# Kernel tuning notes

Measured on AMD Instinct MI355X. Metric: run time of the kernel, lower is better.

## Reference

```python
import jax, jax.numpy as jnp
import numpy as np

DIM_HEAD = 64
NB_FEATURES = 256
COND_LEN = 128
NUM_CHUNKS = 128  # torch .chunk(128, dim=-2) -> 128 chunks
KERNEL_EPS = 1e-4
ATTN_EPS = 1e-6


def gaussian_orthogonal_random_matrix(key, nb_rows, nb_cols):
    # scaling == 0 branch of the torch code
    nb_full = nb_rows // nb_cols
    blocks = []
    for i in range(nb_full + (1 if nb_rows % nb_cols else 0)):
        g = jax.random.normal(jax.random.fold_in(key, i), (nb_cols, nb_cols), dtype=jnp.float32)
        qm, _ = jnp.linalg.qr(g)
        blocks.append(qm.T)
    final = jnp.concatenate(blocks, axis=0)[:nb_rows]
    mult = jnp.linalg.norm(
        jax.random.normal(jax.random.fold_in(key, 10_000), (nb_rows, nb_cols), dtype=jnp.float32), axis=1)
    return mult[:, None] * final  # diag(mult) @ final


def softmax_kernel(x, proj, is_query):
    d = x.shape[-1]
    data_normalizer = d ** (-0.25)
    ratio = proj.shape[0] ** (-0.5)
    # [b,h,n,m]
    data_dash = jnp.einsum('bhnd,md->bhnm', data_normalizer * x, proj)
    diag = (x * x).sum(-1) * 0.5 * (data_normalizer ** 2)  # [b,h,n]
    diag = diag[..., None]
    if is_query:
        m = jnp.max(data_dash, axis=-1, keepdims=True)
    else:
        m = jnp.max(data_dash)
    return ratio * (jnp.exp(data_dash - diag - m) + KERNEL_EPS)


def causal_linear_attention(qf, kf, v):
    b, h, s, m = qf.shape
    e = v.shape[-1]
    # conditioning prefix: non-causal linear attention
    cq, ck, cv = qf[:, :, :COND_LEN], kf[:, :, :COND_LEN], v[:, :, :COND_LEN]
    cond_k_sum = ck.sum(axis=-2)                                   # [b,h,m]
    cond_Dinv = 1.0 / jnp.einsum('bhnd,bhd->bhn', cq, cond_k_sum)
    cond_ctx = jnp.einsum('bhnd,bhne->bhde', ck, cv)               # [b,h,m,e]
    cond_out = jnp.einsum('bhde,bhnd,bhn->bhne', cond_ctx, cq, cond_Dinv)

    # causal chunked recurrence over the remainder
    rest = s - COND_LEN
    L = rest // NUM_CHUNKS
    def to_chunks(t):
        return t[:, :, COND_LEN:].reshape(b, h, NUM_CHUNKS, L, t.shape[-1]).transpose(2, 0, 1, 3, 4)
    qr, kr, vr = to_chunks(qf), to_chunks(kf), to_chunks(v)

    def step(carry, qkv):
        last_k, last_ctx = carry  # [b,h,m], [b,h,m,e]
        qc, kc, vc = qkv          # [b,h,L,m], [b,h,L,m], [b,h,L,e]
        k_cumsum = last_k[:, :, None, :] + jnp.cumsum(kc, axis=-2)
        D_inv = 1.0 / jnp.einsum('bhld,bhld->bhl', qc, k_cumsum + ATTN_EPS)
        ctx = jnp.einsum('bhld,bhle->bhlde', kc, vc)
        ctx_cumsum = last_ctx[:, :, None] + jnp.cumsum(ctx, axis=-3)
        out = jnp.einsum('bhlde,bhld,bhl->bhle', ctx_cumsum, qc, D_inv)
        return (k_cumsum[:, :, -1], ctx_cumsum[:, :, -1]), out

    _, outs = jax.lax.scan(step, (cond_k_sum, cond_ctx), (qr, kr, vr))
    outs = outs.transpose(1, 2, 0, 3, 4).reshape(b, h, rest, e)
    return jnp.concatenate([cond_out, outs], axis=2)


def setup_inputs() -> dict:
    key = jax.random.key(0)
    kq, kk, kv, kp = jax.random.split(key, 4)
    B, H, S = 4, 16, 4096
    q = jax.random.normal(kq, (B, H, S, DIM_HEAD), dtype=jnp.float32)
    k = jax.random.normal(kk, (B, H, S, DIM_HEAD), dtype=jnp.float32)
    v = jax.random.normal(kv, (B, H, S, DIM_HEAD), dtype=jnp.float32)
    projection_matrix = gaussian_orthogonal_random_matrix(kp, NB_FEATURES, DIM_HEAD)
    return {"q": q, "k": k, "v": v, "projection_matrix": projection_matrix}


def reference(q, k, v, projection_matrix):
    qf = softmax_kernel(q, projection_matrix, is_query=True)
    kf = softmax_kernel(k, projection_matrix, is_query=False)
    return causal_linear_attention(qf, kf, v)
```

## Files before the change

kernel.cpp:

```cpp
#include <hip/hip_runtime.h>
#include <math.h>


#define S_TOT 4096
#define CONDL 128
#define SLOT_F 16640
#define RATIO 0.0625f
#define DNORM 0.35355339059327378f
#define KEPS  1e-4f
#define AEPS  1e-6f

typedef __attribute__((ext_vector_type(8))) short bf16x8;
typedef __attribute__((ext_vector_type(4))) short short4v;
typedef __attribute__((ext_vector_type(4))) float f32x4;

#define MFMA16(a,b,c) __builtin_amdgcn_mfma_f32_16x16x32_bf16(a,b,c,0,0,0)

static __device__ __forceinline__ unsigned short f2bh(float x){
    unsigned u = __float_as_uint(x);
    u += 0x7fffu + ((u >> 16) & 1u);
    return (unsigned short)(u >> 16);
}
static __device__ __forceinline__ float bh2f(unsigned short h){
    return __uint_as_float((unsigned)h << 16);
}
static __device__ __forceinline__ unsigned packhl(float x){
    unsigned short h = f2bh(x);
    unsigned short l = f2bh(x - bh2f(h));
    return (unsigned)h | ((unsigned)l << 16);
}
static __device__ __forceinline__ float unpackhl(unsigned u){
    return bh2f((unsigned short)(u & 0xffffu)) + bh2f((unsigned short)(u >> 16));
}
static __device__ __forceinline__ void unpk(const uint4 a, const uint4 b, bf16x8& h, bf16x8& l){
    h[0]=(short)a.x; h[1]=(short)a.y; h[2]=(short)a.z; h[3]=(short)a.w;
    h[4]=(short)b.x; h[5]=(short)b.y; h[6]=(short)b.z; h[7]=(short)b.w;
    l[0]=(short)(a.x>>16); l[1]=(short)(a.y>>16); l[2]=(short)(a.z>>16); l[3]=(short)(a.w>>16);
    l[4]=(short)(b.x>>16); l[5]=(short)(b.y>>16); l[6]=(short)(b.z>>16); l[7]=(short)(b.w>>16);
}
static __device__ __forceinline__ unsigned mapf(float x){
    unsigned u = __float_as_uint(x);
    return (u & 0x80000000u) ? ~u : (u | 0x80000000u);
}
static __device__ __forceinline__ float unmapf(unsigned u){
    return __uint_as_float((u & 0x80000000u) ? (u ^ 0x80000000u) : ~u);
}

static __device__ __forceinline__ void conv_write(const float* __restrict__ Xg, long r0,
        int tid, short (*Xh)[64][8], short (*Xl)[64][8], float* __restrict__ diag_)
{
    int row = tid >> 4;
    int c4  = (tid & 15) * 4;
    float4 x4 = *(const float4*)(Xg + (r0 + row)*64 + c4);
    float xv[4] = {x4.x*DNORM, x4.y*DNORM, x4.z*DNORM, x4.w*DNORM};
    float ss = xv[0]*xv[0] + xv[1]*xv[1] + xv[2]*xv[2] + xv[3]*xv[3];
    ss += __shfl_xor(ss, 1, 64);
    ss += __shfl_xor(ss, 2, 64);
    ss += __shfl_xor(ss, 4, 64);
    ss += __shfl_xor(ss, 8, 64);
    if ((tid & 15) == 0) diag_[row] = 0.5f * ss;
    int rt = row >> 4, lr = row & 15;
    int kk = c4 >> 5, c5 = c4 & 31;
    int fg, j0;
    if (c5 < 16){ fg = c5 >> 2; j0 = 0; } else { fg = (c5 - 16) >> 2; j0 = 4; }
    int f = kk*2 + rt;
    short4v hv, lv;
#pragma unroll
    for (int j=0;j<4;j++){
        unsigned short h = f2bh(xv[j]);
        hv[j] = (short)h;
        lv[j] = (short)f2bh(xv[j] - bh2f(h));
    }
    *(short4v*)&Xh[f][fg*16 + lr][j0] = hv;
    *(short4v*)&Xl[f][fg*16 + lr][j0] = lv;
}

static __device__ __forceinline__ void dd_frags(const short (*Xh)[64][8], const short (*Xl)[64][8],
        int lane, const bf16x8 (&Pfh)[2][2], const bf16x8 (&Pfl)[2][2], f32x4 (&acc)[2][2])
{
#pragma unroll
    for (int rt=0;rt<2;rt++)
#pragma unroll
      for (int mt=0;mt<2;mt++) acc[rt][mt] = f32x4{0.f,0.f,0.f,0.f};
#pragma unroll
    for (int kk=0;kk<2;kk++)
#pragma unroll
      for (int rt=0;rt<2;rt++){
        bf16x8 xh = *(const bf16x8*)&Xh[kk*2+rt][lane][0];
        bf16x8 xl = *(const bf16x8*)&Xl[kk*2+rt][lane][0];
#pragma unroll
        for (int mt=0;mt<2;mt++){
            acc[rt][mt] = MFMA16(xh, Pfh[mt][kk], acc[rt][mt]);
            acc[rt][mt] = MFMA16(xh, Pfl[mt][kk], acc[rt][mt]);
            acc[rt][mt] = MFMA16(xl, Pfh[mt][kk], acc[rt][mt]);
        }
      }
}

static __device__ __forceinline__ void load_pfrags(const unsigned short* __restrict__ Ph,
        const unsigned short* __restrict__ Pl, int w, int l15, int g,
        bf16x8 (&Pfh)[2][2], bf16x8 (&Pfl)[2][2])
{
#pragma unroll
    for (int mt=0; mt<2; mt++)
#pragma unroll
      for (int kk=0; kk<2; kk++){
        const unsigned short* ph = Ph + (w*32 + mt*16 + l15)*64 + kk*32 + g*4;
        const unsigned short* pl = Pl + (w*32 + mt*16 + l15)*64 + kk*32 + g*4;
        bf16x8 fh, fl;
#pragma unroll
        for (int j=0;j<4;j++){
            fh[j]=(short)ph[j]; fh[4+j]=(short)ph[16+j];
            fl[j]=(short)pl[j]; fl[4+j]=(short)pl[16+j];
        }
        Pfh[mt][kk]=fh; Pfl[mt][kk]=fl;
      }
}

__global__ __launch_bounds__(256) void init_p_kernel(const float* __restrict__ proj,
        unsigned short* __restrict__ Ph, unsigned short* __restrict__ Pl){
    int i = blockIdx.x*256 + threadIdx.x;
    float x = proj[i];
    unsigned short h = f2bh(x);
    Ph[i] = h;
    Pl[i] = f2bh(x - bh2f(h));
}

__global__ __launch_bounds__(256) void kmax_kernel(const float* __restrict__ k,
        const unsigned short* __restrict__ Ph, unsigned* __restrict__ kmax_u){
    __shared__ float red[4];
    int tid = threadIdx.x;
    int lane = tid & 63, w = tid >> 6;
    int l15 = lane & 15, g = lane >> 4;
    long r0 = (long)blockIdx.x * 32;
    bf16x8 xh[2][2];
#pragma unroll
    for (int kk=0;kk<2;kk++)
#pragma unroll
      for (int rt=0;rt<2;rt++){
        const float* rp = k + (r0 + rt*16 + l15)*64 + kk*32 + g*4;
        float4 a = *(const float4*)rp;
        float4 b = *(const float4*)(rp + 16);
        float xs[8] = {a.x,a.y,a.z,a.w,b.x,b.y,b.z,b.w};
#pragma unroll
        for (int j=0;j<8;j++) xh[kk][rt][j] = (short)f2bh(xs[j]*DNORM);
      }
    float mx = -1e30f;
#pragma unroll
    for (int mtl=0; mtl<4; mtl++){
        int mtile = w*4 + mtl;
        bf16x8 pf[2];
#pragma unroll
        for (int kk=0;kk<2;kk++){
            const unsigned short* ph = Ph + (mtile*16 + l15)*64 + kk*32 + g*4;
#pragma unroll
            for (int j=0;j<4;j++){ pf[kk][j]=(short)ph[j]; pf[kk][4+j]=(short)ph[16+j]; }
        }
        f32x4 acc[2] = {f32x4{0.f,0.f,0.f,0.f}, f32x4{0.f,0.f,0.f,0.f}};
#pragma unroll
        for (int kk=0;kk<2;kk++)
#pragma unroll
          for (int rt=0;rt<2;rt++)
            acc[rt] = MFMA16(xh[kk][rt], pf[kk], acc[rt]);
#pragma unroll
        for (int rt=0;rt<2;rt++)
#pragma unroll
          for (int i=0;i<4;i++) mx = fmaxf(mx, acc[rt][i]);
    }
#pragma unroll
    for (int d=1; d<64; d<<=1) mx = fmaxf(mx, __shfl_xor(mx, d, 64));
    if (lane == 0) red[w] = mx;
    __syncthreads();
    if (tid == 0){
        float m2 = fmaxf(fmaxf(red[0],red[1]), fmaxf(red[2],red[3]));
        atomicMax(kmax_u, mapf(m2));
    }
}

__global__ __launch_bounds__(512, 4) void b_kernel(const float* __restrict__ k,
        const float* __restrict__ v,
        const unsigned short* __restrict__ Ph, const unsigned short* __restrict__ Pl,
        const unsigned* __restrict__ kmax_u, float* __restrict__ states,
        int CH, int nch){
    __shared__ short Xh[4][64][8], Xl[4][64][8];
    __shared__ unsigned kf_mt[256][36];
    __shared__ unsigned Vt_u[64][36];
    __shared__ float diagk_[32];
    int tid = threadIdx.x;
    int lane = tid & 63, w = tid >> 6;
    int l15 = lane & 15, g = lane >> 4;
    int cx = blockIdx.x, bh = blockIdx.y;
    int o = (cx == 0) ? 0 : CONDL + (cx-1)*CH;
    int nsub = ((cx == 0) ? CONDL : CH) >> 5;
    long rowbase = (long)bh * S_TOT + o;
    float kmax = unmapf(*kmax_u);
    bf16x8 Pfh[2][2], Pfl[2][2];
    load_pfrags(Ph, Pl, w, l15, g, Pfh, Pfl);
    f32x4 Sacc[2][4];
#pragma unroll
    for (int mt=0;mt<2;mt++)
#pragma unroll
      for (int et=0;et<4;et++) Sacc[mt][et] = f32x4{0.f,0.f,0.f,0.f};
    float zacc[2] = {0.f, 0.f};

    for (int st = 0; st < nsub; st++){
        long r0 = rowbase + st*32;
        conv_write(k, r0, tid, Xh, Xl, diagk_);
        {
            int t = tid >> 4, e4 = (tid & 15)*4;
            float4 v4 = *(const float4*)(v + (r0 + t)*64 + e4);
            Vt_u[e4+0][t] = packhl(v4.x);
            Vt_u[e4+1][t] = packhl(v4.y);
            Vt_u[e4+2][t] = packhl(v4.z);
            Vt_u[e4+3][t] = packhl(v4.w);
        }
        __syncthreads();
        f32x4 dk[2][2];
        dd_frags(Xh, Xl, lane, Pfh, Pfl, dk);
        float zd[2] = {0.f, 0.f};
#pragma unroll
        for (int rt=0;rt<2;rt++)
#pragma unroll
          for (int i=0;i<4;i++){
            int t = rt*16 + g*4 + i;
            float dg = diagk_[t];
#pragma unroll
            for (int mt=0;mt<2;mt++){
                float kv = RATIO * (__expf(dk[rt][mt][i] - dg - kmax) + KEPS);
                kf_mt[w*32 + mt*16 + l15][t] = packhl(kv);
                zd[mt] += kv;
            }
          }
#pragma unroll
        for (int mt=0;mt<2;mt++){
            zd[mt] += __shfl_xor(zd[mt], 16, 64);
            zd[mt] += __shfl_xor(zd[mt], 32, 64);
            zacc[mt] += zd[mt];
        }
        __syncthreads();
#pragma unroll
        for (int mt=0;mt<2;mt++){
            int m = (w*2 + mt)*16 + l15;
            const uint4* kp0 = (const uint4*)&kf_mt[m][g*4];
            const uint4* kp1 = (const uint4*)&kf_mt[m][16 + g*4];
            bf16x8 kh, kl; unpk(*kp0, *kp1, kh, kl);
#pragma unroll
            for (int et=0;et<4;et++){
                const uint4* vp0 = (const uint4*)&Vt_u[et*16 + l15][g*4];
                const uint4* vp1 = (const uint4*)&Vt_u[et*16 + l15][16 + g*4];
                bf16x8 vh, vl; unpk(*vp0, *vp1, vh, vl);
                Sacc[mt][et] = MFMA16(kh, vh, Sacc[mt][et]);
                Sacc[mt][et] = MFMA16(kh, vl, Sacc[mt][et]);
                Sacc[mt][et] = MFMA16(kl, vh, Sacc[mt][et]);
            }
        }
        __syncthreads();
    }
    float* Sg = states + ((long)(bh*nch + cx)) * SLOT_F;
#pragma unroll
    for (int mt=0;mt<2;mt++)
#pragma unroll
      for (int et=0;et<4;et++)
#pragma unroll
        for (int i=0;i<4;i++)
            Sg[((w*2+mt)*16 + g*4 + i)*64 + et*16 + l15] = Sacc[mt][et][i];
    if (g == 0){
        Sg[16384 + w*32 + l15]      = zacc[0];
        Sg[16384 + w*32 + 16 + l15] = zacc[1];
    }
}

__global__ __launch_bounds__(256) void scan_kernel(float* __restrict__ states, int nch){
    int idx = blockIdx.x*256 + threadIdx.x;
    if (idx >= SLOT_F) return;
    float* base = states + (long)blockIdx.y * nch * SLOT_F + idx;
    float prev = 0.f;
    for (int c = 0; c < nch; c++){
        float t = base[(long)c * SLOT_F];
        base[(long)c * SLOT_F] = prev;
        prev += t;
    }
}

__global__ __launch_bounds__(512, 2) void d_kernel(const float* __restrict__ q,
        const float* __restrict__ k, const float* __restrict__ v,
        const unsigned short* __restrict__ Ph, const unsigned short* __restrict__ Pl,
        const unsigned* __restrict__ kmax_u, const float* __restrict__ states,
        float* __restrict__ out, int CH, int nch){
    __shared__ short Xh[4][64][8], Xl[4][64][8];
    __shared__ unsigned Sb_u[64][260];
    __shared__ unsigned qf_u[32][260];
    __shared__ unsigned kf_mt[256][36];
    __shared__ unsigned Vt_u[64][36];
    __shared__ unsigned A_u[32][36];
    __shared__ float z_l[256];
    __shared__ float diagq_[32], diagk_[32];
    __shared__ unsigned rmax_u[32];
    __shared__ float den_[32];

    int tid = threadIdx.x;
    int lane = tid & 63, w = tid >> 6;
    int l15 = lane & 15, g = lane >> 4;
    int cx = blockIdx.x, bh = blockIdx.y;
    bool causal = (cx > 0);
    int o = causal ? (CONDL + (cx-1)*CH) : 0;
    int nsub = (causal ? CH : CONDL) >> 5;
    float epsv = causal ? AEPS : 0.f;
    int slot = causal ? cx : 1;
    const float* Sg = states + ((long)(bh*nch + slot)) * SLOT_F;
    long rowbase = (long)bh * S_TOT + o;
    float kmax = unmapf(*kmax_u);

    for (int i = tid; i < 256*16; i += 512){
        int m = i >> 4, e4 = (i & 15)*4;
        float4 s4 = *(const float4*)(Sg + m*64 + e4);
        Sb_u[e4+0][m] = packhl(s4.x);
        Sb_u[e4+1][m] = packhl(s4.y);
        Sb_u[e4+2][m] = packhl(s4.z);
        Sb_u[e4+3][m] = packhl(s4.w);
    }
    if (tid < 256) z_l[tid] = Sg[16384 + tid];
    bf16x8 Pfh[2][2], Pfl[2][2];
    load_pfrags(Ph, Pl, w, l15, g, Pfh, Pfl);

    f32x4 delta[4][4];
    for (int st = 0; st < nsub; st++){
        long r0 = rowbase + st*32;
        if (causal && st > 0 && w >= 4){
            int wv = w - 4;
#pragma unroll
            for (int Mt=0; Mt<4; Mt++)
#pragma unroll
              for (int et=0; et<4; et++){
                int e = et*16 + l15;
                int m0 = (wv*4 + Mt)*16 + g*4;
                uint4* p = (uint4*)&Sb_u[e][m0];
                uint4 cur = *p;
                f32x4 d0 = delta[Mt][et];
                cur.x = packhl(unpackhl(cur.x) + d0[0]);
                cur.y = packhl(unpackhl(cur.y) + d0[1]);
                cur.z = packhl(unpackhl(cur.z) + d0[2]);
                cur.w = packhl(unpackhl(cur.w) + d0[3]);
                *p = cur;
              }
        }
        conv_write(q, r0, tid, Xh, Xl, diagq_);
        if (causal){
            int t = tid >> 4, e4 = (tid & 15)*4;
            float4 v4 = *(const float4*)(v + (r0 + t)*64 + e4);
            Vt_u[e4+0][t] = packhl(v4.x);
            Vt_u[e4+1][t] = packhl(v4.y);
            Vt_u[e4+2][t] = packhl(v4.z);
            Vt_u[e4+3][t] = packhl(v4.w);
        }
        if (tid < 32){ den_[tid] = 0.f; rmax_u[tid] = 0u; }
        __syncthreads();
        f32x4 dq[2][2];
        dd_frags(Xh, Xl, lane, Pfh, Pfl, dq);
#pragma unroll
        for (int rt=0;rt<2;rt++)
#pragma unroll
          for (int i=0;i<4;i++){
            float mx = fmaxf(dq[rt][0][i], dq[rt][1][i]);
            mx = fmaxf(mx, __shfl_xor(mx, 1, 64));
            mx = fmaxf(mx, __shfl_xor(mx, 2, 64));
            mx = fmaxf(mx, __shfl_xor(mx, 4, 64));
            mx = fmaxf(mx, __shfl_xor(mx, 8, 64));
            if (l15 == 0) atomicMax(&rmax_u[rt*16 + g*4 + i], mapf(mx));
          }
        __syncthreads();
        {
            float zc[2]; zc[0] = z_l[w*32 + l15]; zc[1] = z_l[w*32 + 16 + l15];
#pragma unroll
            for (int rt=0;rt<2;rt++)
#pragma unroll
              for (int i=0;i<4;i++){
                int row = rt*16 + g*4 + i;
                float dg = diagq_[row];
                float rm = unmapf(rmax_u[row]);
                float s1p = 0.f, s2p = 0.f;
#pragma unroll
                for (int mt=0;mt<2;mt++){
                    float qv = RATIO * (__expf(dq[rt][mt][i] - dg - rm) + KEPS);
                    s1p += qv; s2p += qv * zc[mt];
                    qf_u[row][w*32 + mt*16 + l15] = packhl(qv);
                }
#pragma unroll
                for (int d=1; d<16; d<<=1){
                    s1p += __shfl_xor(s1p, d, 64);
                    s2p += __shfl_xor(s2p, d, 64);
                }
                if (l15 == 0) atomicAdd(&den_[row], s2p + epsv * s1p);
              }
        }
        if (causal) conv_write(k, r0, tid, Xh, Xl, diagk_);
        __syncthreads();
        float zd[2] = {0.f, 0.f};
        if (causal){
            f32x4 dk[2][2];
            dd_frags(Xh, Xl, lane, Pfh, Pfl, dk);
#pragma unroll
            for (int rt=0;rt<2;rt++)
#pragma unroll
              for (int i=0;i<4;i++){
                int t = rt*16 + g*4 + i;
                float dg = diagk_[t];
#pragma unroll
                for (int mt=0;mt<2;mt++){
                    float kv = RATIO * (__expf(dk[rt][mt][i] - dg - kmax) + KEPS);
                    kf_mt[w*32 + mt*16 + l15][t] = packhl(kv);
                    zd[mt] += kv;
                }
              }
#pragma unroll
            for (int mt=0;mt<2;mt++){
                zd[mt] += __shfl_xor(zd[mt], 16, 64);
                zd[mt] += __shfl_xor(zd[mt], 32, 64);
            }
        }
        __syncthreads();
        if (causal){
            if (g == 0){
                z_l[w*32 + l15]      += zd[0];
                z_l[w*32 + 16 + l15] += zd[1];
            }
            if (w < 4){
                int rt = w >> 1, tt = w & 1;
                f32x4 c0{0.f,0.f,0.f,0.f}, c1{0.f,0.f,0.f,0.f}, c2{0.f,0.f,0.f,0.f};
#pragma unroll
                for (int kt=0; kt<8; kt++){
                    const uint4* qp0 = (const uint4*)&qf_u[rt*16 + l15][kt*32 + g*4];
                    const uint4* qp1 = (const uint4*)&qf_u[rt*16 + l15][kt*32 + 16 + g*4];
                    bf16x8 qh, ql; unpk(*qp0, *qp1, qh, ql);
                    bf16x8 kh, kl;
#pragma unroll
                    for (int p2=0;p2<2;p2++)
#pragma unroll
                      for (int j=0;j<4;j++){
                        unsigned u = kf_mt[kt*32 + p2*16 + g*4 + j][tt*16 + l15];
                        kh[p2*4+j] = (short)u;
                        kl[p2*4+j] = (short)(u >> 16);
                      }
                    c0 = MFMA16(qh, kh, c0);
                    c1 = MFMA16(qh, kl, c1);
                    c2 = MFMA16(ql, kh, c2);
                }
                int t = tt*16 + l15;
#pragma unroll
                for (int i=0;i<4;i++){
                    int r = rt*16 + g*4 + i;
                    float a = c0[i] + c1[i] + c2[i];
                    a = (t <= r) ? a : 0.f;
                    A_u[r][t] = packhl(a);
                    float p = a;
#pragma unroll
                    for (int d=1; d<16; d<<=1) p += __shfl_xor(p, d, 64);
                    if (l15 == 0) atomicAdd(&den_[r], p);
                }
            } else {
                int wv = w - 4;
                bf16x8 vh[4], vl[4];
#pragma unroll
                for (int et=0;et<4;et++){
                    const uint4* vp0 = (const uint4*)&Vt_u[et*16 + l15][g*4];
                    const uint4* vp1 = (const uint4*)&Vt_u[et*16 + l15][16 + g*4];
                    unpk(*vp0, *vp1, vh[et], vl[et]);
                }
#pragma unroll
                for (int Mt=0; Mt<4; Mt++){
                    int m = (wv*4 + Mt)*16 + l15;
                    const uint4* kp0 = (const uint4*)&kf_mt[m][g*4];
                    const uint4* kp1 = (const uint4*)&kf_mt[m][16 + g*4];
                    bf16x8 kh, kl; unpk(*kp0, *kp1, kh, kl);
#pragma unroll
                    for (int et=0; et<4; et++){
                        f32x4 d0{0.f,0.f,0.f,0.f};
                        d0 = MFMA16(kh, vh[et], d0);
                        d0 = MFMA16(kh, vl[et], d0);
                        d0 = MFMA16(kl, vh[et], d0);
                        delta[Mt][et] = d0;
                    }
                }
            }
        }
        __syncthreads();
        {
            int rt = w >> 2, et = w & 3;
            f32x4 c0{0.f,0.f,0.f,0.f}, c1{0.f,0.f,0.f,0.f}, c2{0.f,0.f,0.f,0.f};
#pragma unroll
            for (int kt=0; kt<8; kt++){
                const uint4* qp0 = (const uint4*)&qf_u[rt*16 + l15][kt*32 + g*4];
                const uint4* qp1 = (const uint4*)&qf_u[rt*16 + l15][kt*32 + 16 + g*4];
                bf16x8 qh, ql; unpk(*qp0, *qp1, qh, ql);
                const uint4* sp0 = (const uint4*)&Sb_u[et*16 + l15][kt*32 + g*4];
                const uint4* sp1 = (const uint4*)&Sb_u[et*16 + l15][kt*32 + 16 + g*4];
                bf16x8 sh, sl; unpk(*sp0, *sp1, sh, sl);
                c0 = MFMA16(qh, sh, c0);
                c1 = MFMA16(qh, sl, c1);
                c2 = MFMA16(ql, sh, c2);
            }
            if (causal){
                const uint4* ap0 = (const uint4*)&A_u[rt*16 + l15][g*4];
                const uint4* ap1 = (const uint4*)&A_u[rt*16 + l15][16 + g*4];
                bf16x8 ah, al; unpk(*ap0, *ap1, ah, al);
                const uint4* vp0 = (const uint4*)&Vt_u[et*16 + l15][g*4];
                const uint4* vp1 = (const uint4*)&Vt_u[et*16 + l15][16 + g*4];
                bf16x8 vvh, vvl; unpk(*vp0, *vp1, vvh, vvl);
                c0 = MFMA16(ah, vvh, c0);
                c1 = MFMA16(ah, vvl, c1);
                c2 = MFMA16(al, vvh, c2);
            }
#pragma unroll
            for (int i=0;i<4;i++){
                int row = rt*16 + g*4 + i;
                float oo = (c0[i] + c1[i] + c2[i]) / den_[row];
                out[(r0 + row)*64 + et*16 + l15] = oo;
            }
        }
        __syncthreads();
    }
}

extern "C" void kernel_launch(void* const* d_in, const int* in_sizes, int n_in,
                              void* d_out, int out_size, void* d_ws, size_t ws_size,
                              hipStream_t stream) {
    const float* q = (const float*)d_in[0];
    const float* k = (const float*)d_in[1];
    const float* v = (const float*)d_in[2];
    const float* proj = (const float*)d_in[3];
    float* out = (float*)d_out;

    unsigned* kmax_u = (unsigned*)d_ws;
    unsigned short* Ph = (unsigned short*)((char*)d_ws + 256);
    unsigned short* Pl = Ph + 16384;
    float* states = (float*)((char*)d_ws + 256 + 65536);
    size_t fixed = 256 + 65536;

    int CH, nch;
    size_t need128 = fixed + (size_t)64 * 32 * SLOT_F * 4;
    if (ws_size >= need128){ CH = 128; nch = 32; }
    else                  { CH = 992; nch = 5;  }

    hipMemsetAsync(d_ws, 0, 4, stream);
    hipLaunchKernelGGL(init_p_kernel, dim3(64), dim3(256), 0, stream, proj, Ph, Pl);
    hipLaunchKernelGGL(kmax_kernel, dim3(8192), dim3(256), 0, stream, k, Ph, kmax_u);
    hipLaunchKernelGGL(b_kernel, dim3(nch, 64), dim3(512), 0, stream, k, v, Ph, Pl, kmax_u, states, CH, nch);
    hipLaunchKernelGGL(scan_kernel, dim3(65, 64), dim3(256), 0, stream, states, nch);
    hipLaunchKernelGGL(d_kernel, dim3(nch, 64), dim3(512), 0, stream, q, k, v, Ph, Pl, kmax_u, states, out, CH, nch);
}
```

Baseline: 704.0 us.

## Keep running state in MFMA accumulators and shrink LDS in d_kernel

Result: slower. 1.094 ms (+55.3%).

```diff
diff --git a/kernel.cpp b/kernel.cpp
--- a/kernel.cpp
+++ b/kernel.cpp
@@ -11,10 +11,18 @@
 #define AEPS  1e-6f
 
 typedef __attribute__((ext_vector_type(8))) short bf16x8;
-typedef __attribute__((ext_vector_type(4))) short short4v;
+typedef __attribute__((ext_vector_type(2))) unsigned uint2v;
 typedef __attribute__((ext_vector_type(4))) float f32x4;
 
 #define MFMA16(a,b,c) __builtin_amdgcn_mfma_f32_16x16x32_bf16(a,b,c,0,0,0)
+
+static __device__ __forceinline__ unsigned cvtpk(float a, float b){
+    unsigned r;
+    asm("v_cvt_pk_bf16_f32 %0, %1, %2" : "=v"(r) : "v"(a), "v"(b));
+    return r;
+}
+static __device__ __forceinline__ float lo16f(unsigned u){ return __uint_as_float(u << 16); }
+static __device__ __forceinline__ float hi16f(unsigned u){ return __uint_as_float(u & 0xffff0000u); }
 
 static __device__ __forceinline__ unsigned short f2bh(float x){
     unsigned u = __float_as_uint(x);
@@ -25,12 +33,9 @@
     return __uint_as_float((unsigned)h << 16);
 }
 static __device__ __forceinline__ unsigned packhl(float x){
-    unsigned short h = f2bh(x);
-    unsigned short l = f2bh(x - bh2f(h));
-    return (unsigned)h | ((unsigned)l << 16);
-}
-static __device__ __forceinline__ float unpackhl(unsigned u){
-    return bh2f((unsigned short)(u & 0xffffu)) + bh2f((unsigned short)(u >> 16));
+    unsigned u1 = cvtpk(x, x);
+    float r = x - lo16f(u1);
+    return cvtpk(x, r);
 }
 static __device__ __forceinline__ void unpk(const uint4 a, const uint4 b, bf16x8& h, bf16x8& l){
     h[0]=(short)a.x; h[1]=(short)a.y; h[2]=(short)a.z; h[3]=(short)a.w;
@@ -52,8 +57,8 @@
     int row = tid >> 4;
     int c4  = (tid & 15) * 4;
     float4 x4 = *(const float4*)(Xg + (r0 + row)*64 + c4);
-    float xv[4] = {x4.x*DNORM, x4.y*DNORM, x4.z*DNORM, x4.w*DNORM};
-    float ss = xv[0]*xv[0] + xv[1]*xv[1] + xv[2]*xv[2] + xv[3]*xv[3];
+    float x0 = x4.x*DNORM, x1 = x4.y*DNORM, x2 = x4.z*DNORM, x3 = x4.w*DNORM;
+    float ss = x0*x0 + x1*x1 + x2*x2 + x3*x3;
     ss += __shfl_xor(ss, 1, 64);
     ss += __shfl_xor(ss, 2, 64);
     ss += __shfl_xor(ss, 4, 64);
@@ -64,15 +69,34 @@
     int fg, j0;
     if (c5 < 16){ fg = c5 >> 2; j0 = 0; } else { fg = (c5 - 16) >> 2; j0 = 4; }
     int f = kk*2 + rt;
-    short4v hv, lv;
-#pragma unroll
-    for (int j=0;j<4;j++){
-        unsigned short h = f2bh(xv[j]);
-        hv[j] = (short)h;
-        lv[j] = (short)f2bh(xv[j] - bh2f(h));
-    }
-    *(short4v*)&Xh[f][fg*16 + lr][j0] = hv;
-    *(short4v*)&Xl[f][fg*16 + lr][j0] = lv;
+    unsigned a01 = cvtpk(x0, x1), a23 = cvtpk(x2, x3);
+    unsigned b01 = cvtpk(x0 - lo16f(a01), x1 - hi16f(a01));
+    unsigned b23 = cvtpk(x2 - lo16f(a23), x3 - hi16f(a23));
+    uint2v hv, lv;
+    hv[0] = a01; hv[1] = a23;
+    lv[0] = b01; lv[1] = b23;
+    *(uint2v*)&Xh[f][fg*16 + lr][j0] = hv;
+    *(uint2v*)&Xl[f][fg*16 + lr][j0] = lv;
+}
+
+static __device__ __forceinline__ void load_pfrags(const unsigned short* __restrict__ Ph,
+        const unsigned short* __restrict__ Pl, int w, int l15, int g,
+        bf16x8 (&Pfh)[2][2], bf16x8 (&Pfl)[2][2])
+{
+#pragma unroll
+    for (int mt=0; mt<2; mt++)
+#pragma unroll
+      for (int kk=0; kk<2; kk++){
+        const unsigned short* ph = Ph + (w*32 + mt*16 + l15)*64 + kk*32 + g*4;
+        const unsigned short* pl = Pl + (w*32 + mt*16 + l15)*64 + kk*32 + g*4;
+        bf16x8 fh, fl;
+#pragma unroll
+        for (int j=0;j<4;j++){
+            fh[j]=(short)ph[j]; fh[4+j]=(short)ph[16+j];
+            fl[j]=(short)pl[j]; fl[4+j]=(short)pl[16+j];
+        }
+        Pfh[mt][kk]=fh; Pfl[mt][kk]=fl;
+      }
 }
 
 static __device__ __forceinline__ void dd_frags(const short (*Xh)[64][8], const short (*Xl)[64][8],
@@ -97,33 +121,64 @@
       }
 }
 
-static __device__ __forceinline__ void load_pfrags(const unsigned short* __restrict__ Ph,
-        const unsigned short* __restrict__ Pl, int w, int l15, int g,
-        bf16x8 (&Pfh)[2][2], bf16x8 (&Pfl)[2][2])
+static __device__ __forceinline__ void dd_frags_g(const short (*Xh)[64][8], const short (*Xl)[64][8],
+        int lane, int w, const unsigned short* __restrict__ Pfh, const unsigned short* __restrict__ Pfl,
+        f32x4 (&acc)[2][2])
 {
 #pragma unroll
-    for (int mt=0; mt<2; mt++)
-#pragma unroll
-      for (int kk=0; kk<2; kk++){
-        const unsigned short* ph = Ph + (w*32 + mt*16 + l15)*64 + kk*32 + g*4;
-        const unsigned short* pl = Pl + (w*32 + mt*16 + l15)*64 + kk*32 + g*4;
-        bf16x8 fh, fl;
-#pragma unroll
-        for (int j=0;j<4;j++){
-            fh[j]=(short)ph[j]; fh[4+j]=(short)ph[16+j];
-            fl[j]=(short)pl[j]; fl[4+j]=(short)pl[16+j];
-        }
-        Pfh[mt][kk]=fh; Pfl[mt][kk]=fl;
-      }
+    for (int rr=0;rr<2;rr++)
+#pragma unroll
+      for (int mt=0;mt<2;mt++) acc[rr][mt] = f32x4{0.f,0.f,0.f,0.f};
+#pragma unroll
+    for (int kk=0;kk<2;kk++){
+        bf16x8 ph[2], pl[2];
+#pragma unroll
+        for (int mt=0;mt<2;mt++){
+            int f = w*4 + kk*2 + mt;
+            ph[mt] = *(const bf16x8*)(Pfh + (f*64 + lane)*8);
+            pl[mt] = *(const bf16x8*)(Pfl + (f*64 + lane)*8);
+        }
+#pragma unroll
+        for (int rr=0;rr<2;rr++){
+            bf16x8 xh = *(const bf16x8*)&Xh[kk*2+rr][lane][0];
+            bf16x8 xl = *(const bf16x8*)&Xl[kk*2+rr][lane][0];
+#pragma unroll
+            for (int mt=0;mt<2;mt++){
+                acc[rr][mt] = MFMA16(xh, ph[mt], acc[rr][mt]);
+                acc[rr][mt] = MFMA16(xh, pl[mt], acc[rr][mt]);
+                acc[rr][mt] = MFMA16(xl, ph[mt], acc[rr][mt]);
+            }
+        }
+    }
+}
+
+static __device__ __forceinline__ void sfrag(const f32x4 a, const f32x4 b, bf16x8& h, bf16x8& l){
+    union U { bf16x8 v; unsigned u[4]; } H, L;
+    H.u[0] = cvtpk(a[0], a[1]); H.u[1] = cvtpk(a[2], a[3]);
+    H.u[2] = cvtpk(b[0], b[1]); H.u[3] = cvtpk(b[2], b[3]);
+    L.u[0] = cvtpk(a[0] - lo16f(H.u[0]), a[1] - hi16f(H.u[0]));
+    L.u[1] = cvtpk(a[2] - lo16f(H.u[1]), a[3] - hi16f(H.u[1]));
+    L.u[2] = cvtpk(b[0] - lo16f(H.u[2]), b[1] - hi16f(H.u[2]));
+    L.u[3] = cvtpk(b[2] - lo16f(H.u[3]), b[3] - hi16f(H.u[3]));
+    h = H.v; l = L.v;
 }
 
 __global__ __launch_bounds__(256) void init_p_kernel(const float* __restrict__ proj,
-        unsigned short* __restrict__ Ph, unsigned short* __restrict__ Pl){
+        unsigned short* __restrict__ Ph, unsigned short* __restrict__ Pl,
+        unsigned short* __restrict__ Pfh, unsigned short* __restrict__ Pfl){
     int i = blockIdx.x*256 + threadIdx.x;
     float x = proj[i];
     unsigned short h = f2bh(x);
+    unsigned short l = f2bh(x - bh2f(h));
     Ph[i] = h;
-    Pl[i] = f2bh(x - bh2f(h));
+    Pl[i] = l;
+    int m = i >> 6, d = i & 63;
+    int w = m >> 5, mt = (m >> 4) & 1, l15 = m & 15;
+    int kk = d >> 5, r5 = d & 31;
+    int half = r5 >> 4, g = (r5 & 15) >> 2, jj = r5 & 3;
+    int f = w*4 + kk*2 + mt, lane = g*16 + l15, j = half*4 + jj;
+    int o = (f*64 + lane)*8 + j;
+    Pfh[o] = h; Pfl[o] = l;
 }
 
 __global__ __launch_bounds__(256) void kmax_kernel(const float* __restrict__ k,
@@ -282,25 +337,28 @@
     }
 }
 
-__global__ __launch_bounds__(512, 2) void d_kernel(const float* __restrict__ q,
+__global__ __launch_bounds__(512, 4) void d_kernel(const float* __restrict__ q,
         const float* __restrict__ k, const float* __restrict__ v,
-        const unsigned short* __restrict__ Ph, const unsigned short* __restrict__ Pl,
+        const unsigned short* __restrict__ Pfh, const unsigned short* __restrict__ Pfl,
         const unsigned* __restrict__ kmax_u, const float* __restrict__ states,
         float* __restrict__ out, int CH, int nch){
-    __shared__ short Xh[4][64][8], Xl[4][64][8];
-    __shared__ unsigned Sb_u[64][260];
-    __shared__ unsigned qf_u[32][260];
-    __shared__ unsigned kf_mt[256][36];
-    __shared__ unsigned Vt_u[64][36];
-    __shared__ unsigned A_u[32][36];
-    __shared__ float z_l[256];
-    __shared__ float diagq_[32], diagk_[32];
-    __shared__ unsigned rmax_u[32];
-    __shared__ float den_[32];
+    __shared__ __attribute__((aligned(16))) unsigned lds_[18496];
+    unsigned* qf_ = lds_;
+    unsigned* kf_ = lds_ + 8192;
+    unsigned* XA_ = lds_ + 16384;
+    float*   den_ = (float*)(lds_ + 18432);
+    float*   dgk_ = (float*)(lds_ + 18464);
+    float*   dgq_ = (float*)kf_;
+    unsigned* rmax_ = kf_ + 32;
+    unsigned* A_ = XA_;
+    short (*Xh)[64][8] = (short (*)[64][8])XA_;
+    short (*Xl)[64][8] = (short (*)[64][8])(XA_ + 1024);
 
     int tid = threadIdx.x;
     int lane = tid & 63, w = tid >> 6;
     int l15 = lane & 15, g = lane >> 4;
+    int et = w & 3, rt = w >> 2;
+    bool aowner = (et < 2);
     int cx = blockIdx.x, bh = blockIdx.y;
     bool causal = (cx > 0);
     int o = causal ? (CONDL + (cx-1)*CH) : 0;
@@ -310,212 +368,192 @@
     const float* Sg = states + ((long)(bh*nch + slot)) * SLOT_F;
     long rowbase = (long)bh * S_TOT + o;
     float kmax = unmapf(*kmax_u);
-
-    for (int i = tid; i < 256*16; i += 512){
-        int m = i >> 4, e4 = (i & 15)*4;
-        float4 s4 = *(const float4*)(Sg + m*64 + e4);
-        Sb_u[e4+0][m] = packhl(s4.x);
-        Sb_u[e4+1][m] = packhl(s4.y);
-        Sb_u[e4+2][m] = packhl(s4.z);
-        Sb_u[e4+3][m] = packhl(s4.w);
-    }
-    if (tid < 256) z_l[tid] = Sg[16384 + tid];
-    bf16x8 Pfh[2][2], Pfl[2][2];
-    load_pfrags(Ph, Pl, w, l15, g, Pfh, Pfl);
-
-    f32x4 delta[4][4];
+    int xsw = (l15 & 7) << 2;
+
+    f32x4 S[16];
+#pragma unroll
+    for (int Mt=0; Mt<16; Mt++){
+#pragma unroll
+        for (int i=0;i<4;i++)
+            S[Mt][i] = Sg[(Mt*16 + g*4 + i)*64 + et*16 + l15];
+    }
+    float z0 = Sg[16384 + w*32 + l15];
+    float z1 = Sg[16384 + w*32 + 16 + l15];
+
     for (int st = 0; st < nsub; st++){
         long r0 = rowbase + st*32;
-        if (causal && st > 0 && w >= 4){
-            int wv = w - 4;
-#pragma unroll
-            for (int Mt=0; Mt<4; Mt++)
-#pragma unroll
-              for (int et=0; et<4; et++){
-                int e = et*16 + l15;
-                int m0 = (wv*4 + Mt)*16 + g*4;
-                uint4* p = (uint4*)&Sb_u[e][m0];
-                uint4 cur = *p;
-                f32x4 d0 = delta[Mt][et];
-                cur.x = packhl(unpackhl(cur.x) + d0[0]);
-                cur.y = packhl(unpackhl(cur.y) + d0[1]);
-                cur.z = packhl(unpackhl(cur.z) + d0[2]);
-                cur.w = packhl(unpackhl(cur.w) + d0[3]);
-                *p = cur;
-              }
-        }
-        conv_write(q, r0, tid, Xh, Xl, diagq_);
-        if (causal){
-            int t = tid >> 4, e4 = (tid & 15)*4;
-            float4 v4 = *(const float4*)(v + (r0 + t)*64 + e4);
-            Vt_u[e4+0][t] = packhl(v4.x);
-            Vt_u[e4+1][t] = packhl(v4.y);
-            Vt_u[e4+2][t] = packhl(v4.z);
-            Vt_u[e4+3][t] = packhl(v4.w);
-        }
-        if (tid < 32){ den_[tid] = 0.f; rmax_u[tid] = 0u; }
+        conv_write(q, r0, tid, Xh, Xl, dgq_);
+        if (tid < 32){ den_[tid] = 0.f; rmax_[tid] = 0u; }
         __syncthreads();
         f32x4 dq[2][2];
-        dd_frags(Xh, Xl, lane, Pfh, Pfl, dq);
-#pragma unroll
-        for (int rt=0;rt<2;rt++)
+        dd_frags_g(Xh, Xl, lane, w, Pfh, Pfl, dq);
+#pragma unroll
+        for (int rr=0;rr<2;rr++)
 #pragma unroll
           for (int i=0;i<4;i++){
-            float mx = fmaxf(dq[rt][0][i], dq[rt][1][i]);
+            float mx = fmaxf(dq[rr][0][i], dq[rr][1][i]);
             mx = fmaxf(mx, __shfl_xor(mx, 1, 64));
             mx = fmaxf(mx, __shfl_xor(mx, 2, 64));
             mx = fmaxf(mx, __shfl_xor(mx, 4, 64));
             mx = fmaxf(mx, __shfl_xor(mx, 8, 64));
-            if (l15 == 0) atomicMax(&rmax_u[rt*16 + g*4 + i], mapf(mx));
+            if (l15 == 0) atomicMax(&rmax_[rr*16 + g*4 + i], mapf(mx));
           }
         __syncthreads();
         {
-            float zc[2]; zc[0] = z_l[w*32 + l15]; zc[1] = z_l[w*32 + 16 + l15];
-#pragma unroll
-            for (int rt=0;rt<2;rt++)
+#pragma unroll
+            for (int rr=0;rr<2;rr++)
 #pragma unroll
               for (int i=0;i<4;i++){
-                int row = rt*16 + g*4 + i;
-                float dg = diagq_[row];
-                float rm = unmapf(rmax_u[row]);
+                int row = rr*16 + g*4 + i;
+                float dgv = dgq_[row];
+                float rm = unmapf(rmax_[row]);
                 float s1p = 0.f, s2p = 0.f;
 #pragma unroll
                 for (int mt=0;mt<2;mt++){
-                    float qv = RATIO * (__expf(dq[rt][mt][i] - dg - rm) + KEPS);
-                    s1p += qv; s2p += qv * zc[mt];
-                    qf_u[row][w*32 + mt*16 + l15] = packhl(qv);
+                    float qv = RATIO * (__expf(dq[rr][mt][i] - dgv - rm) + KEPS);
+                    s1p += qv;
+                    s2p += qv * (mt ? z1 : z0);
+                    int m = w*32 + mt*16 + l15;
+                    qf_[row*256 + (m ^ ((row & 7) << 2))] = packhl(qv);
                 }
 #pragma unroll
-                for (int d=1; d<16; d<<=1){
-                    s1p += __shfl_xor(s1p, d, 64);
-                    s2p += __shfl_xor(s2p, d, 64);
+                for (int d2=1; d2<16; d2<<=1){
+                    s1p += __shfl_xor(s1p, d2, 64);
+                    s2p += __shfl_xor(s2p, d2, 64);
                 }
                 if (l15 == 0) atomicAdd(&den_[row], s2p + epsv * s1p);
               }
         }
-        if (causal) conv_write(k, r0, tid, Xh, Xl, diagk_);
-        __syncthreads();
-        float zd[2] = {0.f, 0.f};
+        if (causal) conv_write(k, r0, tid, Xh, Xl, dgk_);
+        __syncthreads();
         if (causal){
             f32x4 dk[2][2];
-            dd_frags(Xh, Xl, lane, Pfh, Pfl, dk);
-#pragma unroll
-            for (int rt=0;rt<2;rt++)
-#pragma unroll
-              for (int i=0;i<4;i++){
-                int t = rt*16 + g*4 + i;
-                float dg = diagk_[t];
+            dd_frags_g(Xh, Xl, lane, w, Pfh, Pfl, dk);
+            float zd0 = 0.f, zd1 = 0.f;
+#pragma unroll
+            for (int rr=0;rr<2;rr++){
+                float dg0 = dgk_[rr*16 + g*4 + 0];
+                float dg1 = dgk_[rr*16 + g*4 + 1];
+                float dg2 = dgk_[rr*16 + g*4 + 2];
+                float dg3 = dgk_[rr*16 + g*4 + 3];
 #pragma unroll
                 for (int mt=0;mt<2;mt++){
-                    float kv = RATIO * (__expf(dk[rt][mt][i] - dg - kmax) + KEPS);
-                    kf_mt[w*32 + mt*16 + l15][t] = packhl(kv);
-                    zd[mt] += kv;
+                    float k0 = RATIO * (__expf(dk[rr][mt][0] - dg0 - kmax) + KEPS);
+                    float k1 = RATIO * (__expf(dk[rr][mt][1] - dg1 - kmax) + KEPS);
+                    float k2 = RATIO * (__expf(dk[rr][mt][2] - dg2 - kmax) + KEPS);
+                    float k3 = RATIO * (__expf(dk[rr][mt][3] - dg3 - kmax) + KEPS);
+                    if (mt == 0) zd0 += k0+k1+k2+k3; else zd1 += k0+k1+k2+k3;
+                    uint4 kw;
+                    kw.x = packhl(k0); kw.y = packhl(k1);
+                    kw.z = packhl(k2); kw.w = packhl(k3);
+                    int m = w*32 + mt*16 + l15;
+                    *(uint4*)&kf_[m*32 + ((rr*16 + g*4) ^ xsw)] = kw;
                 }
-              }
-#pragma unroll
-            for (int mt=0;mt<2;mt++){
-                zd[mt] += __shfl_xor(zd[mt], 16, 64);
-                zd[mt] += __shfl_xor(zd[mt], 32, 64);
-            }
-        }
-        __syncthreads();
+            }
+            zd0 += __shfl_xor(zd0, 16, 64); zd0 += __shfl_xor(zd0, 32, 64);
+            zd1 += __shfl_xor(zd1, 16, 64); zd1 += __shfl_xor(zd1, 32, 64);
+            z0 += zd0; z1 += zd1;
+        }
+        __syncthreads();
+        float vv[8];
         if (causal){
-            if (g == 0){
-                z_l[w*32 + l15]      += zd[0];
-                z_l[w*32 + 16 + l15] += zd[1];
-            }
-            if (w < 4){
-                int rt = w >> 1, tt = w & 1;
-                f32x4 c0{0.f,0.f,0.f,0.f}, c1{0.f,0.f,0.f,0.f}, c2{0.f,0.f,0.f,0.f};
-#pragma unroll
-                for (int kt=0; kt<8; kt++){
-                    const uint4* qp0 = (const uint4*)&qf_u[rt*16 + l15][kt*32 + g*4];
-                    const uint4* qp1 = (const uint4*)&qf_u[rt*16 + l15][kt*32 + 16 + g*4];
-                    bf16x8 qh, ql; unpk(*qp0, *qp1, qh, ql);
-                    bf16x8 kh, kl;
-#pragma unroll
-                    for (int p2=0;p2<2;p2++)
-#pragma unroll
-                      for (int j=0;j<4;j++){
-                        unsigned u = kf_mt[kt*32 + p2*16 + g*4 + j][tt*16 + l15];
-                        kh[p2*4+j] = (short)u;
-                        kl[p2*4+j] = (short)(u >> 16);
-                      }
-                    c0 = MFMA16(qh, kh, c0);
-                    c1 = MFMA16(qh, kl, c1);
-                    c2 = MFMA16(ql, kh, c2);
-                }
-                int t = tt*16 + l15;
-#pragma unroll
-                for (int i=0;i<4;i++){
-                    int r = rt*16 + g*4 + i;
-                    float a = c0[i] + c1[i] + c2[i];
-                    a = (t <= r) ? a : 0.f;
-                    A_u[r][t] = packhl(a);
-                    float p = a;
-#pragma unroll
-                    for (int d=1; d<16; d<<=1) p += __shfl_xor(p, d, 64);
-                    if (l15 == 0) atomicAdd(&den_[r], p);
-                }
-            } else {
-                int wv = w - 4;
-                bf16x8 vh[4], vl[4];
-#pragma unroll
-                for (int et=0;et<4;et++){
-                    const uint4* vp0 = (const uint4*)&Vt_u[et*16 + l15][g*4];
-                    const uint4* vp1 = (const uint4*)&Vt_u[et*16 + l15][16 + g*4];
-                    unpk(*vp0, *vp1, vh[et], vl[et]);
-                }
-#pragma unroll
-                for (int Mt=0; Mt<4; Mt++){
-                    int m = (wv*4 + Mt)*16 + l15;
-                    const uint4* kp0 = (const uint4*)&kf_mt[m][g*4];
-                    const uint4* kp1 = (const uint4*)&kf_mt[m][16 + g*4];
-                    bf16x8 kh, kl; unpk(*kp0, *kp1, kh, kl);
-#pragma unroll
-                    for (int et=0; et<4; et++){
-                        f32x4 d0{0.f,0.f,0.f,0.f};
-                        d0 = MFMA16(kh, vh[et], d0);
-                        d0 = MFMA16(kh, vl[et], d0);
-                        d0 = MFMA16(kl, vh[et], d0);
-                        delta[Mt][et] = d0;
-                    }
-                }
-            }
-        }
-        __syncthreads();
-        {
-            int rt = w >> 2, et = w & 3;
-            f32x4 c0{0.f,0.f,0.f,0.f}, c1{0.f,0.f,0.f,0.f}, c2{0.f,0.f,0.f,0.f};
-#pragma unroll
-            for (int kt=0; kt<8; kt++){
-                const uint4* qp0 = (const uint4*)&qf_u[rt*16 + l15][kt*32 + g*4];
-                const uint4* qp1 = (const uint4*)&qf_u[rt*16 + l15][kt*32 + 16 + g*4];
-                bf16x8 qh, ql; unpk(*qp0, *qp1, qh, ql);
-                const uint4* sp0 = (const uint4*)&Sb_u[et*16 + l15][kt*32 + g*4];
-                const uint4* sp1 = (const uint4*)&Sb_u[et*16 + l15][kt*32 + 16 + g*4];
-                bf16x8 sh, sl; unpk(*sp0, *sp1, sh, sl);
-                c0 = MFMA16(qh, sh, c0);
-                c1 = MFMA16(qh, sl, c1);
-                c2 = MFMA16(ql, sh, c2);
-            }
-            if (causal){
-                const uint4* ap0 = (const uint4*)&A_u[rt*16 + l15][g*4];
-                const uint4* ap1 = (const uint4*)&A_u[rt*16 + l15][16 + g*4];
-                bf16x8 ah, al; unpk(*ap0, *ap1, ah, al);
-                const uint4* vp0 = (const uint4*)&Vt_u[et*16 + l15][g*4];
-                const uint4* vp1 = (const uint4*)&Vt_u[et*16 + l15][16 + g*4];
-                bf16x8 vvh, vvl; unpk(*vp0, *vp1, vvh, vvl);
-                c0 = MFMA16(ah, vvh, c0);
-                c1 = MFMA16(ah, vvl, c1);
-                c2 = MFMA16(al, vvh, c2);
-            }
+            const float* vb = v + (r0)*64 + et*16 + l15;
+#pragma unroll
+            for (int p2=0;p2<2;p2++)
+#pragma unroll
+              for (int j=0;j<4;j++)
+                vv[p2*4+j] = vb[(p2*16 + g*4 + j)*64];
+        }
+        f32x4 cI{0.f,0.f,0.f,0.f};
+        if (causal && aowner){
+            int tt = et;
+            f32x4 c{0.f,0.f,0.f,0.f};
+            int rowb = (rt*16 + l15)*256;
+#pragma unroll
+            for (int kt=0;kt<8;kt++){
+                uint4 q0 = *(const uint4*)&qf_[rowb + ((kt*32 + g*4) ^ xsw)];
+                uint4 q1 = *(const uint4*)&qf_[rowb + ((kt*32 + 16 + g*4) ^ xsw)];
+                bf16x8 qh, ql; unpk(q0, q1, qh, ql);
+                bf16x8 kh, kl;
+#pragma unroll
+                for (int p2=0;p2<2;p2++)
+#pragma unroll
+                  for (int j=0;j<4;j++){
+                    int m = kt*32 + p2*16 + g*4 + j;
+                    unsigned u = kf_[m*32 + ((tt*16 + l15) ^ ((m & 7) << 2))];
+                    kh[p2*4+j] = (short)u;
+                    kl[p2*4+j] = (short)(u >> 16);
+                  }
+                c = MFMA16(qh, kh, c);
+                c = MFMA16(qh, kl, c);
+                c = MFMA16(ql, kh, c);
+            }
+            int t = tt*16 + l15;
 #pragma unroll
             for (int i=0;i<4;i++){
-                int row = rt*16 + g*4 + i;
-                float oo = (c0[i] + c1[i] + c2[i]) / den_[row];
-                out[(r0 + row)*64 + et*16 + l15] = oo;
-            }
+                int r = rt*16 + g*4 + i;
+                float a = (t <= r) ? c[i] : 0.f;
+                A_[r*32 + (t ^ ((r & 7) << 2))] = packhl(a);
+                float p = a;
+                p += __shfl_xor(p, 1, 64);
+                p += __shfl_xor(p, 2, 64);
+                p += __shfl_xor(p, 4, 64);
+                p += __shfl_xor(p, 8, 64);
+                if (l15 == 0) atomicAdd(&den_[r], p);
+            }
+        } else {
+            int rowb = (rt*16 + l15)*256;
+#pragma unroll
+            for (int kt=0;kt<8;kt++){
+                uint4 q0 = *(const uint4*)&qf_[rowb + ((kt*32 + g*4) ^ xsw)];
+                uint4 q1 = *(const uint4*)&qf_[rowb + ((kt*32 + 16 + g*4) ^ xsw)];
+                bf16x8 qh, ql; unpk(q0, q1, qh, ql);
+                bf16x8 sh, sl; sfrag(S[2*kt], S[2*kt+1], sh, sl);
+                cI = MFMA16(qh, sh, cI);
+                cI = MFMA16(qh, sl, cI);
+                cI = MFMA16(ql, sh, cI);
+            }
+        }
+        __syncthreads();
+        if (causal && aowner){
+            int rowb = (rt*16 + l15)*256;
+#pragma unroll
+            for (int kt=0;kt<8;kt++){
+                uint4 q0 = *(const uint4*)&qf_[rowb + ((kt*32 + g*4) ^ xsw)];
+                uint4 q1 = *(const uint4*)&qf_[rowb + ((kt*32 + 16 + g*4) ^ xsw)];
+                bf16x8 qh, ql; unpk(q0, q1, qh, ql);
+                bf16x8 sh, sl; sfrag(S[2*kt], S[2*kt+1], sh, sl);
+                cI = MFMA16(qh, sh, cI);
+                cI = MFMA16(qh, sl, cI);
+                cI = MFMA16(ql, sh, cI);
+            }
+        }
+        if (causal){
+            f32x4 va{vv[0], vv[1], vv[2], vv[3]};
+            f32x4 vb2{vv[4], vv[5], vv[6], vv[7]};
+            bf16x8 vh, vl; sfrag(va, vb2, vh, vl);
+#pragma unroll
+            for (int Mt=0;Mt<16;Mt++){
+                int mb = (Mt*16 + l15)*32;
+                uint4 k0 = *(const uint4*)&kf_[mb + ((g*4) ^ xsw)];
+                uint4 k1 = *(const uint4*)&kf_[mb + ((16 + g*4) ^ xsw)];
+                bf16x8 kh, kl; unpk(k0, k1, kh, kl);
+                S[Mt] = MFMA16(kh, vh, S[Mt]);
+                S[Mt] = MFMA16(kh, vl, S[Mt]);
+                S[Mt] = MFMA16(kl, vh, S[Mt]);
+            }
+            int rb = (rt*16 + l15)*32;
+            uint4 a0 = *(const uint4*)&A_[rb + ((g*4) ^ xsw)];
+            uint4 a1 = *(const uint4*)&A_[rb + ((16 + g*4) ^ xsw)];
+            bf16x8 ah, al; unpk(a0, a1, ah, al);
+            cI = MFMA16(ah, vh, cI);
+            cI = MFMA16(ah, vl, cI);
+            cI = MFMA16(al, vh, cI);
+        }
+#pragma unroll
+        for (int i=0;i<4;i++){
+            int row = rt*16 + g*4 + i;
+            out[(r0 + row)*64 + et*16 + l15] = cI[i] / den_[row];
         }
         __syncthreads();
     }
@@ -531,10 +569,12 @@
     float* out = (float*)d_out;
 
     unsigned* kmax_u = (unsigned*)d_ws;
-    unsigned short* Ph = (unsigned short*)((char*)d_ws + 256);
-    unsigned short* Pl = Ph + 16384;
-    float* states = (float*)((char*)d_ws + 256 + 65536);
-    size_t fixed = 256 + 65536;
+    unsigned short* Ph  = (unsigned short*)((char*)d_ws + 256);
+    unsigned short* Pl  = Ph + 16384;
+    unsigned short* Pfh = Pl + 16384;
+    unsigned short* Pfl = Pfh + 16384;
+    float* states = (float*)((char*)d_ws + 256 + 131072);
+    size_t fixed = 256 + 131072;
 
     int CH, nch;
     size_t need128 = fixed + (size_t)64 * 32 * SLOT_F * 4;
@@ -542,9 +582,9 @@
     else                  { CH = 992; nch = 5;  }
 
     hipMemsetAsync(d_ws, 0, 4, stream);
-    hipLaunchKernelGGL(init_p_kernel, dim3(64), dim3(256), 0, stream, proj, Ph, Pl);
+    hipLaunchKernelGGL(init_p_kernel, dim3(64), dim3(256), 0, stream, proj, Ph, Pl, Pfh, Pfl);
     hipLaunchKernelGGL(kmax_kernel, dim3(8192), dim3(256), 0, stream, k, Ph, kmax_u);
     hipLaunchKernelGGL(b_kernel, dim3(nch, 64), dim3(512), 0, stream, k, v, Ph, Pl, kmax_u, states, CH, nch);
     hipLaunchKernelGGL(scan_kernel, dim3(65, 64), dim3(256), 0, stream, states, nch);
-    hipLaunchKernelGGL(d_kernel, dim3(nch, 64), dim3(512), 0, stream, q, k, v, Ph, Pl, kmax_u, states, out, CH, nch);
-}
+    hipLaunchKernelGGL(d_kernel, dim3(nch, 64), dim3(512), 0, stream, q, k, v, Pfh, Pfl, kmax_u, states, out, CH, nch);
+}
```
